# Kernel tuning notes

Measured on AMD Instinct MI355X. Metric: run time of the kernel, lower is better.

## Reference

```python
import jax, jax.numpy as jnp
import numpy as np


def _forward(embed, enc_Wih, enc_Whh, enc_bih, enc_bhh,
             dec_Wih, dec_Whh, dec_bih, dec_bhh,
             qk_W, qk_b, qv_W, qv_b, ak_W, ak_b,
             out_W, out_b, wd_b,
             hfc1_W, hfc1_b, hfc2_W, hfc2_b,
             cfc1_W, cfc1_b, cfc2_W, cfc2_b,
             src_seqs, src_lengths, trg_seqs):
    B, S = src_seqs.shape
    H = enc_Whh.shape[1]

    # ---- encoder LSTM over packed (masked) source ----
    src_embed = embed[src_seqs]                      # [B,S,D]
    xs = jnp.swapaxes(src_embed, 0, 1)               # [S,B,D]
    step_mask = jnp.arange(S)[:, None] < src_lengths[None, :]  # [S,B]

    def enc_step(carry, inp):
        h, c = carry
        x, m = inp
        z = x @ enc_Wih.T + enc_bih + h @ enc_Whh.T + enc_bhh
        i, f, g, o = jnp.split(z, 4, axis=-1)
        c_new = jax.nn.sigmoid(f) * c + jax.nn.sigmoid(i) * jnp.tanh(g)
        h_new = jax.nn.sigmoid(o) * jnp.tanh(c_new)
        m = m[:, None]
        h_new = jnp.where(m, h_new, h)
        c_new = jnp.where(m, c_new, c)
        out = jnp.where(m, h_new, 0.0)               # pad_packed zero-fills
        return (h_new, c_new), out

    h0 = jnp.zeros((B, H), embed.dtype)
    (hT, cT), enc_outs = jax.lax.scan(enc_step, (h0, h0), (xs, step_mask))
    src_hidden = jnp.swapaxes(enc_outs, 0, 1)        # [B,S,H]

    # ---- init_hidden: MLP transforms of final encoder state ----
    dh = jax.nn.relu(hT @ hfc1_W.T + hfc1_b) @ hfc2_W.T + hfc2_b
    dc = jax.nn.relu(cT @ cfc1_W.T + cfc1_b) @ cfc2_W.T + cfc2_b

    # ---- attention keys/values (constant across decode steps) ----
    q_key = jnp.tanh(src_hidden @ qk_W.T + qk_b)     # [B,S,K]
    q_value = src_hidden @ qv_W.T + qv_b             # [B,S,H]
    attn_mask = jnp.arange(S)[None, :] < src_lengths[:, None]  # [B,S]

    # ---- teacher-forced decode loop (sampling_rate = 1.0) ----
    ans_embed = embed[trg_seqs]                      # [B,T,D]
    dec_inputs = jnp.swapaxes(ans_embed[:, :-1, :], 0, 1)  # [T-1,B,D]

    def dec_step(carry, x):
        h, c = carry
        a_key = jnp.tanh(h @ ak_W.T + ak_b)          # [B,K]
        energy = jnp.einsum('bsk,bk->bs', q_key, a_key)
        energy = jnp.where(attn_mask, energy, -jnp.inf)
        w = jax.nn.softmax(energy, axis=1)           # [B,S]
        context = jnp.einsum('bs,bsh->bh', w, q_value)
        xin = jnp.concatenate([x, context], axis=1)  # [B,D+H]
        z = xin @ dec_Wih.T + dec_bih + h @ dec_Whh.T + dec_bhh
        i, f, g, o = jnp.split(z, 4, axis=-1)
        c_new = jax.nn.sigmoid(f) * c + jax.nn.sigmoid(i) * jnp.tanh(g)
        h_new = jax.nn.sigmoid(o) * jnp.tanh(c_new)
        feat = jnp.concatenate([h_new, context], axis=1) @ out_W.T + out_b  # [B,D]
        logits = feat @ embed.T + wd_b               # tied word_dist, [B,V]
        return (h_new, c_new), logits

    _, outs = jax.lax.scan(dec_step, (dh, dc), dec_inputs)  # [T-1,B,V]
    return jnp.swapaxes(outs, 0, 1)                  # [B,T-1,V]


def setup_inputs() -> dict:
    key = jax.random.key(0)
    ks = jax.random.split(key, 30)
    V, D, H, K = 32000, 512, 1024, 100
    B, S, T = 32, 128, 20

    def w(k, shape):
        return jax.random.normal(k, shape, jnp.float32) * 0.05

    inp = {
        'embed': w(ks[0], (V, D)).at[0].set(0.0),  # padding_idx = 0
        'enc_Wih': w(ks[1], (4 * H, D)), 'enc_Whh': w(ks[2], (4 * H, H)),
        'enc_bih': w(ks[3], (4 * H,)).at[H:2 * H].set(0.0),
        'enc_bhh': w(ks[4], (4 * H,)).at[H:2 * H].set(0.0),
        'dec_Wih': w(ks[5], (4 * H, D + H)), 'dec_Whh': w(ks[6], (4 * H, H)),
        'dec_bih': w(ks[7], (4 * H,)).at[H:2 * H].set(0.0),
        'dec_bhh': w(ks[8], (4 * H,)).at[H:2 * H].set(0.0),
        'qk_W': w(ks[9], (K, H)), 'qk_b': w(ks[10], (K,)),
        'qv_W': w(ks[11], (H, H)), 'qv_b': w(ks[12], (H,)),
        'ak_W': w(ks[13], (K, H)), 'ak_b': w(ks[14], (K,)),
        'out_W': w(ks[15], (D, 2 * H)), 'out_b': w(ks[16], (D,)),
        'wd_b': w(ks[17], (V,)),
        'hfc1_W': w(ks[18], (2 * H, H)), 'hfc1_b': w(ks[19], (2 * H,)),
        'hfc2_W': w(ks[20], (H, 2 * H)), 'hfc2_b': w(ks[21], (H,)),
        'cfc1_W': w(ks[22], (2 * H, H)), 'cfc1_b': w(ks[23], (2 * H,)),
        'cfc2_W': w(ks[24], (H, 2 * H)), 'cfc2_b': w(ks[25], (H,)),
    }
    inp['src_seqs'] = jax.random.randint(ks[26], (B, S), 1, V)
    lens = jnp.sort(jax.random.randint(ks[27], (B,), 1, S + 1))[::-1]
    inp['src_lengths'] = lens.at[0].set(S)  # sorted descending, max = S
    inp['trg_seqs'] = jax.random.randint(ks[28], (B, T), 1, V)
    return inp


def reference(embed, enc_Wih, enc_Whh, enc_bih, enc_bhh,
              dec_Wih, dec_Whh, dec_bih, dec_bhh,
              qk_W, qk_b, qv_W, qv_b, ak_W, ak_b,
              out_W, out_b, wd_b,
              hfc1_W, hfc1_b, hfc2_W, hfc2_b,
              cfc1_W, cfc1_b, cfc2_W, cfc2_b,
              src_seqs, src_lengths, trg_seqs):
    return _forward(embed, enc_Wih, enc_Whh, enc_bih, enc_bhh,
                    dec_Wih, dec_Whh, dec_bih, dec_bhh,
                    qk_W, qk_b, qv_W, qv_b, ak_W, ak_b,
                    out_W, out_b, wd_b,
                    hfc1_W, hfc1_b, hfc2_W, hfc2_b,
                    cfc1_W, cfc1_b, cfc2_W, cfc2_b,
                    src_seqs, src_lengths, trg_seqs)
```

## Files before the change

kernel.cpp:

```cpp
#include <hip/hip_runtime.h>
#include <hip/hip_bf16.h>


using bf16 = __hip_bfloat16;
typedef __attribute__((ext_vector_type(8))) __bf16 bf16x8;
typedef __attribute__((ext_vector_type(4))) float f32x4;

__device__ __forceinline__ bf16x8 ld8(const bf16* p) {
    return *reinterpret_cast<const bf16x8*>(p);
}
__device__ __forceinline__ float b2f(bf16 v) { return __bfloat162float(v); }
__device__ __forceinline__ bf16 f2b(float v) { return __float2bfloat16(v); }
__device__ __forceinline__ unsigned short b2u(bf16 v) {
    unsigned short u; __builtin_memcpy(&u, &v, 2); return u;
}
__device__ __forceinline__ float sigf(float x) { return 1.0f / (1.0f + expf(-x)); }

#define MFMA(a, b, c) __builtin_amdgcn_mfma_f32_16x16x32_bf16((a), (b), (c), 0, 0, 0)

__device__ __forceinline__ void gload_lds16(const bf16* g, bf16* l) {
    __builtin_amdgcn_global_load_lds(
        (const __attribute__((address_space(1))) void*)g,
        (__attribute__((address_space(3))) void*)l, 16, 0, 0);
}

struct ConvDesc { const float* src; bf16* dst; int n; };
struct ConvTable { ConvDesc d[13]; };

__global__ __launch_bounds__(256) void k_conv(ConvTable tab) {
    ConvDesc cd = tab.d[blockIdx.y];
    int stride = gridDim.x * blockDim.x * 4;
    for (int i = (blockIdx.x * blockDim.x + threadIdx.x) * 4; i < cd.n; i += stride) {
        float4 v = *reinterpret_cast<const float4*>(cd.src + i);
        bf16 tmp[4] = {f2b(v.x), f2b(v.y), f2b(v.z), f2b(v.w)};
        *reinterpret_cast<ushort4*>(cd.dst + i) = *reinterpret_cast<const ushort4*>(tmp);
    }
}

__global__ __launch_bounds__(256) void k_gather(const unsigned int* __restrict__ table,
                                                const int* __restrict__ idx,
                                                unsigned int* __restrict__ out) {
    int r = blockIdx.x;
    out[(size_t)r * 256 + threadIdx.x] = table[(size_t)idx[r] * 256 + threadIdx.x];
}

__global__ __launch_bounds__(256) void k_gemm_bt(const bf16* __restrict__ A,
                                                 const bf16* __restrict__ Bw,
                                                 const float* __restrict__ bias,
                                                 float* __restrict__ outF,
                                                 bf16* __restrict__ outB,
                                                 int M, int N, int K, int ldo,
                                                 int ntN, int mode, int xcdmap) {
    __shared__ __attribute__((aligned(16))) bf16 ldsA[128 * 32];
    __shared__ __attribute__((aligned(16))) bf16 ldsB[128 * 32];

    int bx = blockIdx.x;
    int mt, nt;
    if (xcdmap) {
        int ntM = (M + 127) >> 7;
        int x = bx & 7, w = bx >> 3;
        mt = w % ntM;
        nt = (w / ntM) * 8 + x;
        if (nt >= ntN) return;
    } else {
        mt = bx / ntN;
        nt = bx % ntN;
    }
    int tid = threadIdx.x, wv = tid >> 6, l = tid & 63;
    int m0 = mt * 128, n0 = nt * 128;
    int m0w = (wv >> 1) * 64;
    int n0w = (wv & 1) * 64;
    int r = l & 15, ko = l >> 4;

    int srow0 = (l >> 2), suc = l & 3;

    f32x4 zv = {0.f, 0.f, 0.f, 0.f};
    f32x4 acc[4][4];
#pragma unroll
    for (int i = 0; i < 4; ++i)
#pragma unroll
        for (int j = 0; j < 4; ++j) acc[i][j] = zv;

    const bf16x8* LA = (const bf16x8*)ldsA;
    const bf16x8* LB = (const bf16x8*)ldsB;

    for (int kk = 0; kk < K; kk += 32) {
        __syncthreads();
#pragma unroll
        for (int c = 0; c < 2; ++c) {
            int rbase = c * 64 + wv * 16;
            int row = rbase + srow0;
            int gcu = (suc ^ (row & 3)) << 3;
            int arow = m0 + row; if (arow > M - 1) arow = M - 1;
            int brow = n0 + row; if (brow > N - 1) brow = N - 1;
            gload_lds16(A + (size_t)arow * K + kk + gcu, ldsA + rbase * 32);
            gload_lds16(Bw + (size_t)brow * K + kk + gcu, ldsB + rbase * 32);
        }
        __syncthreads();

        bf16x8 af[4], bfv[4];
#pragma unroll
        for (int i = 0; i < 4; ++i) {
            int row = m0w + i * 16 + r;
            af[i] = LA[row * 4 + (ko ^ (row & 3))];
        }
#pragma unroll
        for (int j = 0; j < 4; ++j) {
            int row = n0w + j * 16 + r;
            bfv[j] = LB[row * 4 + (ko ^ (row & 3))];
        }
#pragma unroll
        for (int i = 0; i < 4; ++i)
#pragma unroll
            for (int j = 0; j < 4; ++j) acc[i][j] = MFMA(af[i], bfv[j], acc[i][j]);
    }

    int ccol = l & 15, cr = (l >> 4) * 4;
#pragma unroll
    for (int i = 0; i < 4; ++i) {
#pragma unroll
        for (int j = 0; j < 4; ++j) {
            int n = n0 + n0w + j * 16 + ccol;
            if (n >= N) continue;
            float bv = bias ? bias[n] : 0.f;
#pragma unroll
            for (int q = 0; q < 4; ++q) {
                int row = m0 + m0w + i * 16 + cr + q;
                if (row >= M) continue;
                float v = acc[i][j][q] + bv;
                if (mode == 1) v = tanhf(v);
                if (mode == 2) {
                    outF[((size_t)(row & 31) * 19 + (size_t)(row >> 5)) * 32000 + n] = v;
                } else if (mode == 3) {
                    outB[(size_t)row * ldo + n] = f2b(v);
                } else {
                    outF[(size_t)row * ldo + n] = v;
                }
            }
        }
    }
}

__global__ __launch_bounds__(64) void k_gemm_sm(const bf16* __restrict__ A,
                                                const bf16* __restrict__ W,
                                                const float* __restrict__ bias,
                                                float* __restrict__ outF, int ldof,
                                                bf16* __restrict__ outB, int ldob,
                                                int K, int ntN, int act) {
    int bx = blockIdx.x;
    int mt = bx / ntN, nt = bx % ntN;
    int l = threadIdx.x;
    int r = l & 15, ko = (l >> 4) * 8;
    const bf16* ap = A + (size_t)(mt * 16 + r) * K + ko;
    const bf16* bp = W + (size_t)(nt * 16 + r) * K + ko;
    f32x4 acc = {0.f, 0.f, 0.f, 0.f};
    int nk = K >> 5;
#pragma unroll 4
    for (int kk = 0; kk < nk; ++kk) acc = MFMA(ld8(ap + kk * 32), ld8(bp + kk * 32), acc);
    int n = nt * 16 + (l & 15);
    int cr = (l >> 4) * 4;
    float bv = bias ? bias[n] : 0.f;
#pragma unroll
    for (int q = 0; q < 4; ++q) {
        int row = mt * 16 + cr + q;
        float v = acc[q] + bv;
        if (act == 1) v = fmaxf(v, 0.f);
        if (act == 2) v = tanhf(v);
        if (outF) outF[(size_t)row * ldof + n] = v;
        if (outB) outB[(size_t)row * ldob + n] = f2b(v);
    }
}

__global__ __launch_bounds__(256, 1) void k_enc_all(const bf16* __restrict__ Zx,
                                                    const bf16* __restrict__ Whh,
                                                    const float* __restrict__ bih,
                                                    const float* __restrict__ bhh,
                                                    const int* __restrict__ lens,
                                                    unsigned int* __restrict__ hbw0,
                                                    unsigned int* __restrict__ hbw1,
                                                    bf16* __restrict__ cbT,
                                                    bf16* __restrict__ SH,
                                                    int* __restrict__ flags) {
    __shared__ bf16 hlds[8][1024];
    __shared__ float zl[4][8][16];
    __shared__ unsigned short hpub[8][16];
    unsigned int* hldsw = (unsigned int*)hlds;
    const bf16x8* hldsv = (const bf16x8*)hlds;

    int bid = blockIdx.x;
    int grp = bid >> 6, jblk = bid & 63;
    int j0 = jblk * 16;
    int tid = threadIdx.x;
    int g = tid >> 6, l = tid & 63;
    int r = l & 15, ko = (l >> 4) * 8;

    bf16x8 wreg[32];
    {
        const bf16* wp = Whh + (size_t)(g * 1024 + j0 + r) * 1024 + ko;
#pragma unroll
        for (int kk = 0; kk < 32; ++kk) wreg[kk] = ld8(wp + kk * 32);
    }

    int bl = tid >> 4, ji = tid & 15;
    int b = grp * 8 + bl;
    int j = j0 + ji;
    bool pw = tid < 128;
    float bs[4] = {0.f, 0.f, 0.f, 0.f};
    int lenv = 0;
    float hs = 0.f, cs = 0.f;
    const bf16* zxp = Zx;
    if (pw) {
#pragma unroll
        for (int gg = 0; gg < 4; ++gg) bs[gg] = bih[gg * 1024 + j] + bhh[gg * 1024 + j];
        lenv = lens[b];
        zxp = Zx + (size_t)(b * 128) * 4096 + j;
    }
    int ccol = l & 15, cr = (l >> 4) * 4;
    int rk = r & 7;
    unsigned int gbase = grp * 4096;

    for (int t = 0; t < 128; ++t) {
        float za[4] = {0.f, 0.f, 0.f, 0.f};
        if (pw) {
#pragma unroll
            for (int gg = 0; gg < 4; ++gg)
                za[gg] = b2f(zxp[(size_t)t * 4096 + gg * 1024]);
        }

        if (t > 0) {
            if (tid < 64) {
                const int* fp = flags + (t - 1) * 256 + grp * 64;
                while (true) {
                    int v = __hip_atomic_load(fp + l, __ATOMIC_RELAXED,
                                              __HIP_MEMORY_SCOPE_AGENT);
                    if (__all(v != 0)) break;
                    __builtin_amdgcn_s_sleep(1);
                }
                __builtin_amdgcn_sched_barrier(0);
            }
            __syncthreads();
        }

        const unsigned int* hw = ((t & 1) ? hbw1 : hbw0) + gbase;
#pragma unroll 4
        for (int i = 0; i < 16; ++i) {
            int d = i * 256 + tid;
            int bb = d >> 9, w = d & 511;
            unsigned int v = __hip_atomic_load(hw + d, __ATOMIC_RELAXED,
                                               __HIP_MEMORY_SCOPE_AGENT);
            hldsw[bb * 512 + ((((w >> 2) ^ (bb & 7)) << 2) | (w & 3))] = v;
        }
        __syncthreads();

        f32x4 acc0 = {0.f, 0.f, 0.f, 0.f};
#pragma unroll
        for (int kk = 0; kk < 32; ++kk) {
            int u = kk * 4 + (l >> 4);
            acc0 = MFMA(hldsv[(r & 7) * 128 + (u ^ rk)], wreg[kk], acc0);
        }
        if (l < 32) {
#pragma unroll
            for (int q = 0; q < 4; ++q) zl[g][cr + q][ccol] = acc0[q];
        }
        __syncthreads();

        if (pw) {
            float zi = zl[0][bl][ji] + za[0] + bs[0];
            float zf = zl[1][bl][ji] + za[1] + bs[1];
            float zg = zl[2][bl][ji] + za[2] + bs[2];
            float zo = zl[3][bl][ji] + za[3] + bs[3];
            float cn = sigf(zf) * cs + sigf(zi) * tanhf(zg);
            float hn = sigf(zo) * tanhf(cn);
            bool msk = t < lenv;
            if (msk) { hs = hn; cs = cn; }
            hpub[bl][ji] = b2u(f2b(hs));
            SH[((size_t)b * 128 + t) * 1024 + j] = msk ? f2b(hn) : f2b(0.f);
            if (t == 127) cbT[b * 1024 + j] = f2b(cs);
        }
        __syncthreads();

        unsigned int* hwn = ((t & 1) ? hbw0 : hbw1) + gbase;
        if (tid < 64) {
            int pb = tid >> 3, pq = tid & 7;
            unsigned int val = (unsigned int)hpub[pb][2 * pq] |
                               ((unsigned int)hpub[pb][2 * pq + 1] << 16);
            __hip_atomic_store(hwn + (size_t)pb * 512 + (j0 >> 1) + pq, val,
                               __ATOMIC_RELAXED, __HIP_MEMORY_SCOPE_AGENT);
        }
        __syncthreads();
        if (tid == 0)
            __hip_atomic_fetch_add(flags + t * 256 + grp * 64 + jblk, 1,
                                   __ATOMIC_RELAXED, __HIP_MEMORY_SCOPE_AGENT);
    }
}

__global__ __launch_bounds__(256) void k_attn(const bf16* __restrict__ embedB,
                                              const int* __restrict__ trg,
                                              const bf16* __restrict__ akWB,
                                              const float* __restrict__ akb,
                                              const float* __restrict__ qkB,
                                              const bf16* __restrict__ qvBb,
                                              const int* __restrict__ lens,
                                              const bf16* __restrict__ hb,
                                              bf16* __restrict__ xin,
                                              bf16* __restrict__ featT, int t) {
    int b = blockIdx.x >> 2, chunk = blockIdx.x & 3;
    int tid = threadIdx.x;
    if (chunk == 0) {
        const unsigned int* er = (const unsigned int*)(embedB + (size_t)trg[b * 20 + t] * 512);
        ((unsigned int*)(xin + (size_t)b * 1536))[tid] = er[tid];
    }

    __shared__ float part[256];
    __shared__ float ak[100];
    __shared__ float ew[128];
    __shared__ float mxs, inv_s;

    float s = 0.f;
    if (tid < 200) {
        int n = tid >> 1, hh = tid & 1;
        const bf16* wr = akWB + (size_t)n * 1024 + hh * 512;
        const bf16* hr = hb + (size_t)b * 1024 + hh * 512;
#pragma unroll 8
        for (int k = 0; k < 512; ++k) s += b2f(hr[k]) * b2f(wr[k]);
    }
    part[tid] = s;
    __syncthreads();
    if (tid < 100) ak[tid] = tanhf(part[2 * tid] + part[2 * tid + 1] + akb[tid]);
    __syncthreads();

    if (tid < 128) {
        const float* qr = qkB + ((size_t)b * 128 + tid) * 100;
        float e = 0.f;
#pragma unroll 4
        for (int k = 0; k < 100; ++k) e += qr[k] * ak[k];
        ew[tid] = (tid < lens[b]) ? e : -INFINITY;
    }
    __syncthreads();
    if (tid < 64) {
        float m = fmaxf(ew[tid], ew[tid + 64]);
#pragma unroll
        for (int off = 32; off; off >>= 1) m = fmaxf(m, __shfl_down(m, off));
        if (tid == 0) mxs = m;
    }
    __syncthreads();
    if (tid < 128) ew[tid] = expf(ew[tid] - mxs);
    __syncthreads();
    if (tid < 64) {
        float s2 = ew[tid] + ew[tid + 64];
#pragma unroll
        for (int off = 32; off; off >>= 1) s2 += __shfl_down(s2, off);
        if (tid == 0) inv_s = 1.0f / s2;
    }
    __syncthreads();

    {
        int jj = (chunk << 8) + tid;
        const bf16* qvb = qvBb + ((size_t)b * 128) * 1024 + jj;
        float a0 = 0.f;
#pragma unroll 4
        for (int s3 = 0; s3 < 128; ++s3) a0 += ew[s3] * b2f(qvb[(size_t)s3 * 1024]);
        a0 *= inv_s;
        bf16 cb = f2b(a0);
        xin[(size_t)b * 1536 + 512 + jj] = cb;
        featT[(size_t)b * 2048 + 1024 + jj] = cb;
    }
}

__global__ __launch_bounds__(64) void k_dec_z(const bf16* __restrict__ xin,
                                              const bf16* __restrict__ Wih,
                                              const bf16* __restrict__ hb_in,
                                              const bf16* __restrict__ Whh,
                                              const float* __restrict__ bih,
                                              const float* __restrict__ bhh,
                                              float* __restrict__ cd,
                                              bf16* __restrict__ hb_out,
                                              bf16* __restrict__ featT) {
    __shared__ float zl[32][16];
    int j0 = blockIdx.x * 4;
    int l = threadIdx.x;
    int r = l & 15, ko = (l >> 4) * 8;
    int wrow = (r >> 2) * 1024 + j0 + (r & 3);

    f32x4 acc0 = {0.f, 0.f, 0.f, 0.f}, acc1 = {0.f, 0.f, 0.f, 0.f};
    {
        const bf16* a0 = xin + (size_t)r * 1536 + ko;
        const bf16* a1 = xin + (size_t)(16 + r) * 1536 + ko;
        const bf16* bp = Wih + (size_t)wrow * 1536 + ko;
#pragma unroll 4
        for (int kk = 0; kk < 48; ++kk) {
            bf16x8 bv = ld8(bp + kk * 32);
            acc0 = MFMA(ld8(a0 + kk * 32), bv, acc0);
            acc1 = MFMA(ld8(a1 + kk * 32), bv, acc1);
        }
    }
    {
        const bf16* a0 = hb_in + (size_t)r * 1024 + ko;
        const bf16* a1 = hb_in + (size_t)(16 + r) * 1024 + ko;
        const bf16* bp = Whh + (size_t)wrow * 1024 + ko;
#pragma unroll 4
        for (int kk = 0; kk < 32; ++kk) {
            bf16x8 bv = ld8(bp + kk * 32);
            acc0 = MFMA(ld8(a0 + kk * 32), bv, acc0);
            acc1 = MFMA(ld8(a1 + kk * 32), bv, acc1);
        }
    }
    int ccol = l & 15, cr = (l >> 4) * 4;
#pragma unroll
    for (int q = 0; q < 4; ++q) {
        zl[cr + q][ccol] = acc0[q];
        zl[16 + cr + q][ccol] = acc1[q];
    }
    __syncthreads();

#pragma unroll
    for (int e = l; e < 128; e += 64) {
        int b = e >> 2, jj = e & 3;
        int j = j0 + jj;
        float zi = zl[b][jj]      + bih[j]        + bhh[j];
        float zf = zl[b][4 + jj]  + bih[1024 + j] + bhh[1024 + j];
        float zg = zl[b][8 + jj]  + bih[2048 + j] + bhh[2048 + j];
        float zo = zl[b][12 + jj] + bih[3072 + j] + bhh[3072 + j];
        int hi = b * 1024 + j;
        float co = cd[hi];
        float cn = sigf(zf) * co + sigf(zi) * tanhf(zg);
        float hn = sigf(zo) * tanhf(cn);
        cd[hi] = cn;
        bf16 hnb = f2b(hn);
        hb_out[hi] = hnb;
        featT[(size_t)b * 2048 + j] = hnb;
    }
}

extern "C" void kernel_launch(void* const* d_in, const int* in_sizes, int n_in,
                              void* d_out, int out_size, void* d_ws, size_t ws_size,
                              hipStream_t stream) {
    const float* embed   = (const float*)d_in[0];
    const float* enc_Wih = (const float*)d_in[1];
    const float* enc_Whh = (const float*)d_in[2];
    const float* enc_bih = (const float*)d_in[3];
    const float* enc_bhh = (const float*)d_in[4];
    const float* dec_Wih = (const float*)d_in[5];
    const float* dec_Whh = (const float*)d_in[6];
    const float* dec_bih = (const float*)d_in[7];
    const float* dec_bhh = (const float*)d_in[8];
    const float* qk_W    = (const float*)d_in[9];
    const float* qk_b    = (const float*)d_in[10];
    const float* qv_W    = (const float*)d_in[11];
    const float* qv_b    = (const float*)d_in[12];
    const float* ak_W    = (const float*)d_in[13];
    const float* ak_b    = (const float*)d_in[14];
    const float* out_W   = (const float*)d_in[15];
    const float* out_b   = (const float*)d_in[16];
    const float* wd_b    = (const float*)d_in[17];
    const float* hfc1_W  = (const float*)d_in[18];
    const float* hfc1_b  = (const float*)d_in[19];
    const float* hfc2_W  = (const float*)d_in[20];
    const float* hfc2_b  = (const float*)d_in[21];
    const float* cfc1_W  = (const float*)d_in[22];
    const float* cfc1_b  = (const float*)d_in[23];
    const float* cfc2_W  = (const float*)d_in[24];
    const float* cfc2_b  = (const float*)d_in[25];
    const int* src  = (const int*)d_in[26];
    const int* lens = (const int*)d_in[27];
    const int* trg  = (const int*)d_in[28];

    char* cur = (char*)d_ws;
    auto alloc = [&](size_t bytes) -> char* {
        char* p = cur;
        cur += (bytes + 255) & ~(size_t)255;
        return p;
    };
    bf16* embedB  = (bf16*)alloc((size_t)16384000 * 2);
    bf16* encWihB = (bf16*)alloc((size_t)2097152 * 2);
    bf16* encWhhB = (bf16*)alloc((size_t)4194304 * 2);
    bf16* decWihB = (bf16*)alloc((size_t)6291456 * 2);
    bf16* decWhhB = (bf16*)alloc((size_t)4194304 * 2);
    bf16* qkWB    = (bf16*)alloc((size_t)102400 * 2);
    bf16* qvWB    = (bf16*)alloc((size_t)1048576 * 2);
    bf16* outWB   = (bf16*)alloc((size_t)1048576 * 2);
    bf16* hfc1B   = (bf16*)alloc((size_t)2097152 * 2);
    bf16* hfc2B   = (bf16*)alloc((size_t)2097152 * 2);
    bf16* cfc1B   = (bf16*)alloc((size_t)2097152 * 2);
    bf16* cfc2B   = (bf16*)alloc((size_t)2097152 * 2);
    bf16* akWB    = (bf16*)alloc((size_t)102400 * 2);
    bf16*  Xsrc  = (bf16*)alloc((size_t)4096 * 512 * 2);
    bf16*  Zx    = (bf16*)alloc((size_t)4096 * 4096 * 2);
    bf16*  SH    = (bf16*)alloc((size_t)4096 * 1024 * 2);
    float* qkB   = (float*)alloc((size_t)4096 * 100 * 4);
    bf16*  qvBb  = (bf16*)alloc((size_t)4096 * 1024 * 2);
    bf16*  hbA   = (bf16*)alloc(32 * 1024 * 2);
    bf16*  hbB   = (bf16*)alloc(32 * 1024 * 2);
    bf16*  cbT   = (bf16*)alloc(32 * 1024 * 2);
    bf16*  t1    = (bf16*)alloc(32 * 2048 * 2);
    float* cd    = (float*)alloc(32 * 1024 * 4);
    bf16*  hdA   = (bf16*)alloc(32 * 1024 * 2);
    bf16*  hdB   = (bf16*)alloc(32 * 1024 * 2);
    bf16*  xin   = (bf16*)alloc(32 * 1536 * 2);
    bf16*  featAll = (bf16*)alloc((size_t)608 * 2048 * 2);
    bf16*  feats = (bf16*)alloc((size_t)608 * 512 * 2);
    int*   flags = (int*)alloc((size_t)128 * 256 * 4);
    if ((size_t)(cur - (char*)d_ws) > ws_size) return;

    hipMemsetAsync(hbA, 0, 32 * 1024 * 2, stream);
    hipMemsetAsync(flags, 0, (size_t)128 * 256 * 4, stream);

    ConvTable tab;
    tab.d[0]  = {embed,   embedB,  16384000};
    tab.d[1]  = {enc_Wih, encWihB, 2097152};
    tab.d[2]  = {enc_Whh, encWhhB, 4194304};
    tab.d[3]  = {dec_Wih, decWihB, 6291456};
    tab.d[4]  = {dec_Whh, decWhhB, 4194304};
    tab.d[5]  = {qk_W,    qkWB,    102400};
    tab.d[6]  = {qv_W,    qvWB,    1048576};
    tab.d[7]  = {out_W,   outWB,   1048576};
    tab.d[8]  = {hfc1_W,  hfc1B,   2097152};
    tab.d[9]  = {hfc2_W,  hfc2B,   2097152};
    tab.d[10] = {cfc1_W,  cfc1B,   2097152};
    tab.d[11] = {cfc2_W,  cfc2B,   2097152};
    tab.d[12] = {ak_W,    akWB,    102400};
    k_conv<<<dim3(1024, 13), 256, 0, stream>>>(tab);

    k_gather<<<4096, 256, 0, stream>>>((const unsigned int*)embedB, src, (unsigned int*)Xsrc);

    k_gemm_bt<<<32 * 32, 256, 0, stream>>>(Xsrc, encWihB, nullptr, nullptr, Zx,
                                           4096, 4096, 512, 4096, 32, 3, 0);

    {
        const bf16* ZxA = Zx;  const bf16* WhhA = encWhhB;
        const float* bihA = enc_bih; const float* bhhA = enc_bhh;
        const int* lensA = lens;
        unsigned int* hb0A = (unsigned int*)hbA;
        unsigned int* hb1A = (unsigned int*)hbB;
        bf16* cbTA = cbT; bf16* SHA = SH; int* flagsA = flags;
        void* args[] = {(void*)&ZxA, (void*)&WhhA, (void*)&bihA, (void*)&bhhA,
                        (void*)&lensA, (void*)&hb0A, (void*)&hb1A, (void*)&cbTA,
                        (void*)&SHA, (void*)&flagsA};
        hipLaunchCooperativeKernel((void*)k_enc_all, dim3(256), dim3(256), args, 0, stream);
    }
    bf16* hbT = hbA;

    k_gemm_sm<<<256, 64, 0, stream>>>(hbT, hfc1B, hfc1_b, nullptr, 0, t1, 2048, 1024, 128, 1);
    k_gemm_sm<<<128, 64, 0, stream>>>(t1, hfc2B, hfc2_b, nullptr, 0, hdA, 1024, 2048, 64, 0);
    k_gemm_sm<<<256, 64, 0, stream>>>(cbT, cfc1B, cfc1_b, nullptr, 0, t1, 2048, 1024, 128, 1);
    k_gemm_sm<<<128, 64, 0, stream>>>(t1, cfc2B, cfc2_b, cd, 1024, nullptr, 0, 2048, 64, 0);

    k_gemm_bt<<<32, 256, 0, stream>>>(SH, qkWB, qk_b, qkB, nullptr,
                                      4096, 100, 1024, 100, 1, 1, 0);
    k_gemm_bt<<<256, 256, 0, stream>>>(SH, qvWB, qv_b, nullptr, qvBb,
                                       4096, 1024, 1024, 1024, 8, 3, 0);

    for (int t = 0; t < 19; ++t) {
        const bf16* hin = (t & 1) ? hdB : hdA;
        bf16* hout = (t & 1) ? hdA : hdB;
        bf16* featT = featAll + (size_t)t * 32 * 2048;
        k_attn<<<128, 256, 0, stream>>>(embedB, trg, akWB, ak_b, qkB, qvBb, lens,
                                        hin, xin, featT, t);
        k_dec_z<<<256, 64, 0, stream>>>(xin, decWihB, hin, decWhhB, dec_bih, dec_bhh,
                                        cd, hout, featT);
    }

    k_gemm_bt<<<20, 256, 0, stream>>>(featAll, outWB, out_b, nullptr, feats,
                                      608, 512, 2048, 512, 4, 3, 0);

    k_gemm_bt<<<1280, 256, 0, stream>>>(feats, embedB, wd_b, (float*)d_out, nullptr,
                                        608, 32000, 512, 0, 250, 2, 1);
}
```

Before: 2.051 ms.

## Split decoder step kernels across more waves and blocks for parallelism

The decoder attention kernel now runs on 8 column chunks per batch row instead of 4, splits the value-weighted sum over two halves of the source axis, and reduces the halves through shared memory. The attention-key dot product switches to 8-wide vector loads. The LSTM gate kernel grows from one wave to four waves per block, each handling a quarter of the combined K range, with the partial results summed in LDS. The goal is to shorten the latency-bound per-step kernels in the 19-step sequential loop, at the cost of extra shared-memory reductions and more blocks recomputing the attention softmax.

```diff
diff --git a/kernel.cpp b/kernel.cpp
--- a/kernel.cpp
+++ b/kernel.cpp
@@ -5,6 +5,7 @@
 using bf16 = __hip_bfloat16;
 typedef __attribute__((ext_vector_type(8))) __bf16 bf16x8;
 typedef __attribute__((ext_vector_type(4))) float f32x4;
+typedef __attribute__((ext_vector_type(8))) unsigned short u16x8;
 
 __device__ __forceinline__ bf16x8 ld8(const bf16* p) {
     return *reinterpret_cast<const bf16x8*>(p);
@@ -13,6 +14,10 @@
 __device__ __forceinline__ bf16 f2b(float v) { return __float2bfloat16(v); }
 __device__ __forceinline__ unsigned short b2u(bf16 v) {
     unsigned short u; __builtin_memcpy(&u, &v, 2); return u;
+}
+__device__ __forceinline__ float u2f(unsigned short u) {
+    unsigned int x = (unsigned int)u << 16;
+    float f; __builtin_memcpy(&f, &x, 4); return f;
 }
 __device__ __forceinline__ float sigf(float x) { return 1.0f / (1.0f + expf(-x)); }
 
@@ -304,7 +309,7 @@
                                               const bf16* __restrict__ hb,
                                               bf16* __restrict__ xin,
                                               bf16* __restrict__ featT, int t) {
-    int b = blockIdx.x >> 2, chunk = blockIdx.x & 3;
+    int b = blockIdx.x >> 3, chunk = blockIdx.x & 7;
     int tid = threadIdx.x;
     if (chunk == 0) {
         const unsigned int* er = (const unsigned int*)(embedB + (size_t)trg[b * 20 + t] * 512);
@@ -319,10 +324,14 @@
     float s = 0.f;
     if (tid < 200) {
         int n = tid >> 1, hh = tid & 1;
-        const bf16* wr = akWB + (size_t)n * 1024 + hh * 512;
-        const bf16* hr = hb + (size_t)b * 1024 + hh * 512;
+        const u16x8* wr = (const u16x8*)(akWB + (size_t)n * 1024 + hh * 512);
+        const u16x8* hr = (const u16x8*)(hb + (size_t)b * 1024 + hh * 512);
 #pragma unroll 8
-        for (int k = 0; k < 512; ++k) s += b2f(hr[k]) * b2f(wr[k]);
+        for (int k = 0; k < 64; ++k) {
+            u16x8 wv8 = wr[k], hv8 = hr[k];
+#pragma unroll
+            for (int e = 0; e < 8; ++e) s += u2f(hv8[e]) * u2f(wv8[e]);
+        }
     }
     part[tid] = s;
     __syncthreads();
@@ -355,72 +364,79 @@
     __syncthreads();
 
     {
-        int jj = (chunk << 8) + tid;
-        const bf16* qvb = qvBb + ((size_t)b * 128) * 1024 + jj;
+        int col = tid & 127, sh2 = tid >> 7;
+        int jj = (chunk << 7) + col;
+        const bf16* qvb = qvBb + ((size_t)b * 128 + sh2 * 64) * 1024 + jj;
         float a0 = 0.f;
-#pragma unroll 4
-        for (int s3 = 0; s3 < 128; ++s3) a0 += ew[s3] * b2f(qvb[(size_t)s3 * 1024]);
-        a0 *= inv_s;
-        bf16 cb = f2b(a0);
+#pragma unroll 8
+        for (int s3 = 0; s3 < 64; ++s3)
+            a0 += ew[sh2 * 64 + s3] * b2f(qvb[(size_t)s3 * 1024]);
+        part[tid] = a0;
+    }
+    __syncthreads();
+    if (tid < 128) {
+        int jj = (chunk << 7) + tid;
+        float v = (part[tid] + part[tid + 128]) * inv_s;
+        bf16 cb = f2b(v);
         xin[(size_t)b * 1536 + 512 + jj] = cb;
         featT[(size_t)b * 2048 + 1024 + jj] = cb;
     }
 }
 
-__global__ __launch_bounds__(64) void k_dec_z(const bf16* __restrict__ xin,
-                                              const bf16* __restrict__ Wih,
-                                              const bf16* __restrict__ hb_in,
-                                              const bf16* __restrict__ Whh,
-                                              const float* __restrict__ bih,
-                                              const float* __restrict__ bhh,
-                                              float* __restrict__ cd,
-                                              bf16* __restrict__ hb_out,
-                                              bf16* __restrict__ featT) {
-    __shared__ float zl[32][16];
+__global__ __launch_bounds__(256) void k_dec_z(const bf16* __restrict__ xin,
+                                               const bf16* __restrict__ Wih,
+                                               const bf16* __restrict__ hb_in,
+                                               const bf16* __restrict__ Whh,
+                                               const float* __restrict__ bih,
+                                               const float* __restrict__ bhh,
+                                               float* __restrict__ cd,
+                                               bf16* __restrict__ hb_out,
+                                               bf16* __restrict__ featT) {
+    __shared__ float zp[4][32][16];
     int j0 = blockIdx.x * 4;
-    int l = threadIdx.x;
+    int tid = threadIdx.x;
+    int wv = tid >> 6, l = tid & 63;
     int r = l & 15, ko = (l >> 4) * 8;
     int wrow = (r >> 2) * 1024 + j0 + (r & 3);
 
     f32x4 acc0 = {0.f, 0.f, 0.f, 0.f}, acc1 = {0.f, 0.f, 0.f, 0.f};
-    {
-        const bf16* a0 = xin + (size_t)r * 1536 + ko;
-        const bf16* a1 = xin + (size_t)(16 + r) * 1536 + ko;
-        const bf16* bp = Wih + (size_t)wrow * 1536 + ko;
+    int k0 = wv * 20, k1 = k0 + 20;
 #pragma unroll 4
-        for (int kk = 0; kk < 48; ++kk) {
-            bf16x8 bv = ld8(bp + kk * 32);
-            acc0 = MFMA(ld8(a0 + kk * 32), bv, acc0);
-            acc1 = MFMA(ld8(a1 + kk * 32), bv, acc1);
-        }
-    }
-    {
-        const bf16* a0 = hb_in + (size_t)r * 1024 + ko;
-        const bf16* a1 = hb_in + (size_t)(16 + r) * 1024 + ko;
-        const bf16* bp = Whh + (size_t)wrow * 1024 + ko;
-#pragma unroll 4
-        for (int kk = 0; kk < 32; ++kk) {
-            bf16x8 bv = ld8(bp + kk * 32);
-            acc0 = MFMA(ld8(a0 + kk * 32), bv, acc0);
-            acc1 = MFMA(ld8(a1 + kk * 32), bv, acc1);
-        }
+    for (int k = k0; k < k1; ++k) {
+        const bf16 *a0p, *a1p, *bp;
+        if (k < 48) {
+            a0p = xin + (size_t)r * 1536 + k * 32 + ko;
+            a1p = xin + (size_t)(16 + r) * 1536 + k * 32 + ko;
+            bp = Wih + (size_t)wrow * 1536 + k * 32 + ko;
+        } else {
+            int kh = k - 48;
+            a0p = hb_in + (size_t)r * 1024 + kh * 32 + ko;
+            a1p = hb_in + (size_t)(16 + r) * 1024 + kh * 32 + ko;
+            bp = Whh + (size_t)wrow * 1024 + kh * 32 + ko;
+        }
+        bf16x8 bv = ld8(bp);
+        acc0 = MFMA(ld8(a0p), bv, acc0);
+        acc1 = MFMA(ld8(a1p), bv, acc1);
     }
     int ccol = l & 15, cr = (l >> 4) * 4;
 #pragma unroll
     for (int q = 0; q < 4; ++q) {
-        zl[cr + q][ccol] = acc0[q];
-        zl[16 + cr + q][ccol] = acc1[q];
-    }
-    __syncthreads();
-
-#pragma unroll
-    for (int e = l; e < 128; e += 64) {
-        int b = e >> 2, jj = e & 3;
+        zp[wv][cr + q][ccol] = acc0[q];
+        zp[wv][16 + cr + q][ccol] = acc1[q];
+    }
+    __syncthreads();
+
+    if (tid < 128) {
+        int b = tid >> 2, jj = tid & 3;
         int j = j0 + jj;
-        float zi = zl[b][jj]      + bih[j]        + bhh[j];
-        float zf = zl[b][4 + jj]  + bih[1024 + j] + bhh[1024 + j];
-        float zg = zl[b][8 + jj]  + bih[2048 + j] + bhh[2048 + j];
-        float zo = zl[b][12 + jj] + bih[3072 + j] + bhh[3072 + j];
+        float zi = zp[0][b][jj] + zp[1][b][jj] + zp[2][b][jj] + zp[3][b][jj]
+                   + bih[j] + bhh[j];
+        float zf = zp[0][b][4 + jj] + zp[1][b][4 + jj] + zp[2][b][4 + jj] +
+                   zp[3][b][4 + jj] + bih[1024 + j] + bhh[1024 + j];
+        float zg = zp[0][b][8 + jj] + zp[1][b][8 + jj] + zp[2][b][8 + jj] +
+                   zp[3][b][8 + jj] + bih[2048 + j] + bhh[2048 + j];
+        float zo = zp[0][b][12 + jj] + zp[1][b][12 + jj] + zp[2][b][12 + jj] +
+                   zp[3][b][12 + jj] + bih[3072 + j] + bhh[3072 + j];
         int hi = b * 1024 + j;
         float co = cd[hi];
         float cn = sigf(zf) * co + sigf(zi) * tanhf(zg);
@@ -554,10 +570,10 @@
         const bf16* hin = (t & 1) ? hdB : hdA;
         bf16* hout = (t & 1) ? hdA : hdB;
         bf16* featT = featAll + (size_t)t * 32 * 2048;
-        k_attn<<<128, 256, 0, stream>>>(embedB, trg, akWB, ak_b, qkB, qvBb, lens,
+        k_attn<<<256, 256, 0, stream>>>(embedB, trg, akWB, ak_b, qkB, qvBb, lens,
                                         hin, xin, featT, t);
-        k_dec_z<<<256, 64, 0, stream>>>(xin, decWihB, hin, decWhhB, dec_bih, dec_bhh,
-                                        cd, hout, featT);
+        k_dec_z<<<256, 256, 0, stream>>>(xin, decWihB, hin, decWhhB, dec_bih, dec_bhh,
+                                         cd, hout, featT);
     }
 
     k_gemm_bt<<<20, 256, 0, stream>>>(featAll, outWB, out_b, nullptr, feats,
```

Measured after the change: 1.826 ms. 11.0% less time.
